# Kernel optimization log

Hardware: AMD Instinct MI355X
Metric: run time of the kernel (lower is better)

The kernel has to match this reference:

```python
import jax, jax.numpy as jnp
import numpy as np

NUM_HEADS = 8
ATTN_DIM = 64

def setup_inputs() -> dict:
    key = jax.random.key(0)
    ks = jax.random.split(key, 16)
    C = ATTN_DIM
    inp = {
        "rgb_fea": jax.random.normal(ks[0], (2, C, 48, 48), jnp.float32),
        "depth_fea": jax.random.normal(ks[1], (2, 1, 24, 24), jnp.float32),
        # expend_conv: Conv2d(1 -> C, k=1), with bias (torch default)
        "w_exp": jax.random.normal(ks[2], (C, 1), jnp.float32) * 0.2,
        "b_exp": jax.random.normal(ks[3], (C,), jnp.float32) * 0.02,
        # q/k/v linears (no bias), weights stored torch-style [out, in]
        "w_rgb_q": jax.random.normal(ks[4], (C, C), jnp.float32) * (C ** -0.5),
        "w_rgb_k": jax.random.normal(ks[5], (C, C), jnp.float32) * (C ** -0.5),
        "w_rgb_v": jax.random.normal(ks[6], (C, C), jnp.float32) * (C ** -0.5),
        "w_dep_q": jax.random.normal(ks[7], (C, C), jnp.float32) * (C ** -0.5),
        "w_dep_k": jax.random.normal(ks[8], (C, C), jnp.float32) * (C ** -0.5),
        "w_dep_v": jax.random.normal(ks[9], (C, C), jnp.float32) * (C ** -0.5),
        # output projections (with bias)
        "w_rgb_proj": jax.random.normal(ks[10], (C, C), jnp.float32) * (C ** -0.5),
        "b_rgb_proj": jax.random.normal(ks[11], (C,), jnp.float32) * 0.02,
        "w_dep_proj": jax.random.normal(ks[12], (C, C), jnp.float32) * (C ** -0.5),
        "b_dep_proj": jax.random.normal(ks[13], (C,), jnp.float32) * 0.02,
        # compress_conv: Conv2d(2C -> C, k=1), with bias
        "w_comp": jax.random.normal(ks[14], (C, 2 * C), jnp.float32) * ((2 * C) ** -0.5),
        "b_comp": jax.random.normal(ks[15], (C,), jnp.float32) * 0.02,
    }
    return inp


def _heads(x, b, n, h):
    # [B, N, C] -> [B, H, N, C/H]
    c = x.shape[-1]
    return x.reshape(b, n, h, c // h).transpose(0, 2, 1, 3)


def reference(rgb_fea, depth_fea, w_exp, b_exp,
              w_rgb_q, w_rgb_k, w_rgb_v, w_dep_q, w_dep_k, w_dep_v,
              w_rgb_proj, b_rgb_proj, w_dep_proj, b_dep_proj,
              w_comp, b_comp):
    b, c, h, w = rgb_fea.shape
    H = NUM_HEADS
    scale = (c // H) ** -0.5

    # expend_conv (1x1) + ReLU + bilinear upsample (align_corners=False)
    d = jnp.einsum('bihw,oi->bohw', depth_fea, w_exp) + b_exp[None, :, None, None]
    d = jax.nn.relu(d)
    d = jax.image.resize(d, (b, c, h, w), method='bilinear')

    # (B,C,H,W) -> transpose(1,3) -> (B,W,H,C) -> (B, N=w*h, C)
    N = w * h
    rgb = rgb_fea.transpose(0, 3, 2, 1).reshape(b, N, c)
    dep = d.transpose(0, 3, 2, 1).reshape(b, N, c)

    rq = _heads(rgb @ w_rgb_q.T, b, N, H)
    rk = _heads(rgb @ w_rgb_k.T, b, N, H)
    rv = _heads(rgb @ w_rgb_v.T, b, N, H)
    dq = _heads(dep @ w_dep_q.T, b, N, H)
    dk = _heads(dep @ w_dep_k.T, b, N, H)
    dv = _heads(dep @ w_dep_v.T, b, N, H)

    # rgb queries attend to depth keys/values
    rgb_attn = jax.nn.softmax(jnp.einsum('bhnd,bhmd->bhnm', rq, dk) * scale, axis=-1)
    rgb_out = jnp.einsum('bhnm,bhmd->bhnd', rgb_attn, dv)
    rgb_out = rgb_out.transpose(0, 2, 1, 3).reshape(b, N, c) @ w_rgb_proj.T + b_rgb_proj

    # depth queries attend to rgb keys/values
    dep_attn = jax.nn.softmax(jnp.einsum('bhnd,bhmd->bhnm', dq, rk) * scale, axis=-1)
    dep_out = jnp.einsum('bhnm,bhmd->bhnd', dep_attn, rv)
    dep_out = dep_out.transpose(0, 2, 1, 3).reshape(b, N, c) @ w_dep_proj.T + b_dep_proj

    # (B,N,C) -> (B,C,N) -> (B,C,w,h)
    rgb_out = rgb_out.transpose(0, 2, 1).reshape(b, c, w, h)
    dep_out = dep_out.transpose(0, 2, 1).reshape(b, c, w, h)

    fuse = jnp.concatenate([rgb_out, dep_out], axis=1)
    fuse = jnp.einsum('bihw,oi->bohw', fuse, w_comp) + b_comp[None, :, None, None]
    return jax.nn.gelu(fuse, approximate=False)
```

## Files before the change

kernel.cpp:

```cpp
#include <hip/hip_runtime.h>
#include <math.h>

#define BATCH 2
#define C 64
#define HH 48
#define WW 48
#define NTOK 2304
#define HEADS 8
#define KVSTRIDE 12

typedef unsigned short bf16_t;
typedef __attribute__((ext_vector_type(8))) short bf16x8;
typedef __attribute__((ext_vector_type(4))) float f32x4;

__device__ __forceinline__ bf16_t f2bf(float f) {
    unsigned int u = __float_as_uint(f);
    u = (u + 0x7fffu + ((u >> 16) & 1u)) >> 16;
    return (bf16_t)u;
}
__device__ __forceinline__ unsigned pack2(float a, float b) {
    return (unsigned)f2bf(a) | ((unsigned)f2bf(b) << 16);
}
__device__ __forceinline__ float4 ld_bf4(const bf16_t* p) {
    uint2 v = *(const uint2*)p;
    float4 r;
    r.x = __uint_as_float(v.x << 16); r.y = __uint_as_float(v.x & 0xffff0000u);
    r.z = __uint_as_float(v.y << 16); r.w = __uint_as_float(v.y & 0xffff0000u);
    return r;
}

__device__ __forceinline__ void stage_x_row(
    float* xrow, const float* rgb, const float* dep,
    const float* w_exp, const float* b_exp,
    int b, int n, int strm, int c0, int cstep)
{
    int wi = n / HH, hi = n % HH;
    if (strm == 0) {
        const float* base = rgb + (size_t)b * C * NTOK + (size_t)hi * WW + wi;
        for (int c = c0; c < 64; c += cstep)
            xrow[c] = base[(size_t)c * NTOK];
    } else {
        float cy = 0.5f * hi - 0.25f, cx = 0.5f * wi - 0.25f;
        float fy0 = floorf(cy), fx0 = floorf(cx);
        float fy = cy - fy0, fx = cx - fx0;
        int y0 = max((int)fy0, 0), x0 = max((int)fx0, 0);
        int y1 = min((int)fy0 + 1, 23), x1 = min((int)fx0 + 1, 23);
        const float* dp = dep + b * 576;
        float d00 = dp[y0*24 + x0], d01 = dp[y0*24 + x1];
        float d10 = dp[y1*24 + x0], d11 = dp[y1*24 + x1];
        for (int c = c0; c < 64; c += cstep) {
            float w = w_exp[c], bb = b_exp[c];
            float r00 = fmaxf(w*d00 + bb, 0.f), r01 = fmaxf(w*d01 + bb, 0.f);
            float r10 = fmaxf(w*d10 + bb, 0.f), r11 = fmaxf(w*d11 + bb, 0.f);
            xrow[c] = (1.f-fy)*((1.f-fx)*r00 + fx*r01) + fy*((1.f-fx)*r10 + fx*r11);
        }
    }
}


__global__ __launch_bounds__(256) void wprep_kernel(
    const float* __restrict__ w_rp, const float* __restrict__ w_dp,
    const float* __restrict__ w_comp,
    const float* __restrict__ b_rp, const float* __restrict__ b_dp,
    const float* __restrict__ b_comp,
    float* __restrict__ W1, float* __restrict__ W2, float* __restrict__ beff)
{
    int bx = blockIdx.x, m = blockIdx.y;
    const float* Wp = m ? w_dp : w_rp;
    float* Wo = m ? W2 : W1;
    __shared__ float Wps[64][68];
    int tid = threadIdx.x;
    int sr = tid >> 4, sc4 = (tid & 15) * 4;
    #pragma unroll
    for (int rr = 0; rr < 4; ++rr) {
        int r = rr*16 + sr;
        *(float4*)&Wps[r][sc4] = *(const float4*)&Wp[r*64 + sc4];
    }
    __syncthreads();
    int r = tid >> 4;
    int o = bx*16 + r;
    int c4 = (tid & 15) * 4;
    float a0 = 0, a1 = 0, a2 = 0, a3 = 0;
    for (int j = 0; j < 64; ++j) {
        float wc = w_comp[o*128 + m*64 + j];
        float4 wp = *(const float4*)&Wps[j][c4];
        a0 += wc*wp.x; a1 += wc*wp.y; a2 += wc*wp.z; a3 += wc*wp.w;
    }
    Wo[o*64 + c4]     = a0;
    Wo[o*64 + c4 + 1] = a1;
    Wo[o*64 + c4 + 2] = a2;
    Wo[o*64 + c4 + 3] = a3;
    if (bx == 0 && m == 0 && tid < 64) {
        float s = b_comp[tid];
        for (int j = 0; j < 64; ++j)
            s += w_comp[tid*128 + j] * b_rp[j] + w_comp[tid*128 + 64 + j] * b_dp[j];
        beff[tid] = s;
    }
}

__global__ __launch_bounds__(256) void qkv_kernel(
    const float* __restrict__ rgb, const float* __restrict__ dep,
    const float* __restrict__ w_exp, const float* __restrict__ b_exp,
    const float* __restrict__ w_rq, const float* __restrict__ w_rk, const float* __restrict__ w_rv,
    const float* __restrict__ w_dq, const float* __restrict__ w_dk, const float* __restrict__ w_dv,
    bf16_t* __restrict__ Qb, bf16_t* __restrict__ Kb, bf16_t* __restrict__ VT)
{
    int tile = blockIdx.x;
    int z    = blockIdx.y;
    int b = z >> 1, strm = z & 1;
    int sb = strm*2 + b;

    __shared__ float Xs[64][68];
    __shared__ float Ws[64][68];
    int tid = threadIdx.x;
    {
        int r = tid & 63, c0 = tid >> 6;
        stage_x_row(&Xs[r][0], rgb, dep, w_exp, b_exp, b, tile*64 + r, strm, c0, 4);
    }
    int sr = tid >> 4, sc = (tid & 15) * 4;
    int ty = tid >> 4, tx = tid & 15;

    #pragma unroll
    for (int m = 0; m < 3; ++m) {
        const float* W = strm ? (m == 0 ? w_dq : m == 1 ? w_dk : w_dv)
                              : (m == 0 ? w_rq : m == 1 ? w_rk : w_rv);
        __syncthreads();
        #pragma unroll
        for (int rr = 0; rr < 4; ++rr) {
            int r = rr*16 + sr;
            *(float4*)&Ws[r][sc] = *(const float4*)&W[r*64 + sc];
        }
        __syncthreads();

        float acc[4][4] = {};
        #pragma unroll
        for (int k = 0; k < 64; k += 4) {
            float4 xv[4], wv4[4];
            #pragma unroll
            for (int i = 0; i < 4; ++i) xv[i] = *(const float4*)&Xs[4*ty + i][k];
            #pragma unroll
            for (int j = 0; j < 4; ++j) wv4[j] = *(const float4*)&Ws[tx + 16*j][k];
            #pragma unroll
            for (int i = 0; i < 4; ++i)
                #pragma unroll
                for (int j = 0; j < 4; ++j)
                    acc[i][j] += xv[i].x*wv4[j].x + xv[i].y*wv4[j].y + xv[i].z*wv4[j].z + xv[i].w*wv4[j].w;
        }
        float scale = (m == 0) ? (0.35355339059327373f * 1.4426950408889634f) : 1.0f;
        #pragma unroll
        for (int j = 0; j < 4; ++j) {
            int o = tx + 16*j;
            int h = o >> 3, d = o & 7;
            #pragma unroll
            for (int i = 0; i < 4; ++i) {
                int n = tile*64 + 4*ty + i;
                bf16_t v = f2bf(acc[i][j] * scale);
                if (m == 0)      Qb[(((size_t)sb*8 + h)*NTOK + n)*8 + d] = v;
                else if (m == 1) Kb[(((size_t)sb*8 + h)*NTOK + n)*8 + d] = v;
                else             VT[(((size_t)sb*8 + h)*8 + d)*NTOK + n] = v;
            }
        }
    }
}

__global__ __launch_bounds__(256) void attn_kernel(
    const bf16_t* __restrict__ Qb, const bf16_t* __restrict__ Kb,
    const bf16_t* __restrict__ VT,
    float* __restrict__ AOr, float* __restrict__ AOd)
{
    int h = blockIdx.y;
    int z = blockIdx.z;
    int b = z >> 1, which = z & 1;
    int qsb = which * 2 + b;
    int ksb = (1 - which) * 2 + b;
    const bf16_t* Q  = Qb + ((size_t)qsb * 8 + h) * NTOK * 8;
    const bf16_t* K  = Kb + ((size_t)ksb * 8 + h) * NTOK * 8;
    const bf16_t* Vt = VT + ((size_t)ksb * 8 + h) * 8 * NTOK;
    float* AO = which ? AOd : AOr;

    __shared__ __align__(16) bf16_t Pls[4][16][40];
    __shared__ __align__(16) float  Ols[4][16][16];

    int tid = threadIdx.x;
    int t = tid & 63, w = tid >> 6;
    int m16 = t & 15, quad = t >> 4;
    int qt = blockIdx.x * 4 + w;
    int n0 = qt * 16;

    const bf16x8 zf = {0,0,0,0,0,0,0,0};
    const bf16x8 onesf = {0x3F80,0x3F80,0x3F80,0x3F80,0x3F80,0x3F80,0x3F80,0x3F80};
    const f32x4 cz = {0.f, 0.f, 0.f, 0.f};

    bf16x8 qf = (quad == 0) ? *(const bf16x8*)&Q[(size_t)(n0 + m16) * 8] : zf;

    f32x4 oacc = cz;

    #pragma unroll 1
    for (int ck = 0; ck < 72; ++ck) {
        int k0 = ck * 32;
        bf16x8 kf0 = (quad == 0) ? *(const bf16x8*)&K[(size_t)(k0 + m16) * 8]      : zf;
        bf16x8 kf1 = (quad == 0) ? *(const bf16x8*)&K[(size_t)(k0 + 16 + m16) * 8] : zf;
        bf16x8 vf = (m16 < 8) ? *(const bf16x8*)&Vt[(size_t)m16 * NTOK + k0 + quad * 8]
                  : (m16 == 8 ? onesf : zf);

        f32x4 s0 = __builtin_amdgcn_mfma_f32_16x16x32_bf16(qf, kf0, cz, 0, 0, 0);
        f32x4 s1 = __builtin_amdgcn_mfma_f32_16x16x32_bf16(qf, kf1, cz, 0, 0, 0);

        #pragma unroll
        for (int r = 0; r < 4; ++r) {
            float p0 = __builtin_amdgcn_exp2f(s0[r]);
            float p1 = __builtin_amdgcn_exp2f(s1[r]);
            Pls[w][quad*4 + r][m16]      = (bf16_t)(__float_as_uint(p0) >> 16);
            Pls[w][quad*4 + r][m16 + 16] = (bf16_t)(__float_as_uint(p1) >> 16);
        }
        bf16x8 pf = *(const bf16x8*)&Pls[w][m16][quad * 8];
        oacc = __builtin_amdgcn_mfma_f32_16x16x32_bf16(pf, vf, oacc, 0, 0, 0);
    }

    #pragma unroll
    for (int r = 0; r < 4; ++r)
        Ols[w][quad*4 + r][m16] = oacc[r];
    #pragma unroll
    for (int e = 0; e < 2; ++e) {
        int idx = t * 2 + e;
        int qq = idx >> 3, d = idx & 7;
        float val = Ols[w][qq][d] / Ols[w][qq][8];
        AO[((size_t)b * NTOK + n0 + qq) * 64 + 8 * h + d] = val;
    }
}

__global__ __launch_bounds__(256) void outcomp_kernel(
    const float* __restrict__ AOr, const float* __restrict__ AOd,
    const float* __restrict__ W1, const float* __restrict__ W2,
    const float* __restrict__ beff, float* __restrict__ out)
{
    int tile = blockIdx.x;
    int b    = blockIdx.y;
    int n0 = tile * 32;
    __shared__ float Ar[32][68];
    __shared__ float Ad[32][68];
    __shared__ float W1s[64][68];
    __shared__ float W2s[64][68];
    int tid = threadIdx.x;
    #pragma unroll
    for (int pass = 0; pass < 2; ++pass) {
        int idx = tid + pass*256;
        int row = idx >> 4, c4 = (idx & 15) * 4;
        *(float4*)&Ar[row][c4] = *(const float4*)&AOr[((size_t)b*NTOK + n0 + row)*64 + c4];
        *(float4*)&Ad[row][c4] = *(const float4*)&AOd[((size_t)b*NTOK + n0 + row)*64 + c4];
    }
    {
        int sr = tid >> 4, sc4 = (tid & 15) * 4;
        #pragma unroll
        for (int rr = 0; rr < 4; ++rr) {
            int r = rr*16 + sr;
            *(float4*)&W1s[r][sc4] = *(const float4*)&W1[r*64 + sc4];
            *(float4*)&W2s[r][sc4] = *(const float4*)&W2[r*64 + sc4];
        }
    }
    __syncthreads();

    int tx = tid & 15, ty = tid >> 4;
    float g[2][4] = {};
    #pragma unroll
    for (int k = 0; k < 64; k += 4) {
        float4 xr0 = *(const float4*)&Ar[2*ty][k];
        float4 xr1 = *(const float4*)&Ar[2*ty + 1][k];
        float4 xd0 = *(const float4*)&Ad[2*ty][k];
        float4 xd1 = *(const float4*)&Ad[2*ty + 1][k];
        #pragma unroll
        for (int jj = 0; jj < 4; ++jj) {
            float4 w1 = *(const float4*)&W1s[tx + 16*jj][k];
            float4 w2 = *(const float4*)&W2s[tx + 16*jj][k];
            g[0][jj] += xr0.x*w1.x + xr0.y*w1.y + xr0.z*w1.z + xr0.w*w1.w
                      + xd0.x*w2.x + xd0.y*w2.y + xd0.z*w2.z + xd0.w*w2.w;
            g[1][jj] += xr1.x*w1.x + xr1.y*w1.y + xr1.z*w1.z + xr1.w*w1.w
                      + xd1.x*w2.x + xd1.y*w2.y + xd1.z*w2.z + xd1.w*w2.w;
        }
    }
    #pragma unroll
    for (int jj = 0; jj < 4; ++jj) {
        int o = tx + 16*jj;
        float be = beff[o];
        #pragma unroll
        for (int i = 0; i < 2; ++i) {
            int n = n0 + 2*ty + i;
            int wi = n / HH, hi = n % HH;
            float x = g[i][jj] + be;
            float gl = 0.5f * x * (1.0f + erff(x * 0.70710678118654752f));
            out[((b*C + o)*WW + wi)*HH + hi] = gl;
        }
    }
}

__global__ __launch_bounds__(256) void kv_all_kernel(
    const float* __restrict__ rgb, const float* __restrict__ dep,
    const float* __restrict__ w_exp, const float* __restrict__ b_exp,
    const float* __restrict__ w_rk, const float* __restrict__ w_rv,
    const float* __restrict__ w_dk, const float* __restrict__ w_dv,
    bf16_t* __restrict__ Kr, bf16_t* __restrict__ Vr,
    bf16_t* __restrict__ Kd, bf16_t* __restrict__ Vd)
{
    int tile = blockIdx.x;
    int m    = blockIdx.y;
    int z    = blockIdx.z;
    int b = z >> 1, strm = z & 1;
    const float* W = strm ? (m ? w_dv : w_dk) : (m ? w_rv : w_rk);
    bf16_t* O = (strm ? (m ? Vd : Kd) : (m ? Vr : Kr))
              + ((size_t)b * NTOK + tile * 64) * 64;

    __shared__ float Xs[64][68];
    __shared__ float Ws[64][68];
    int tid = threadIdx.x;
    {
        int r = tid & 63, c0 = tid >> 6;
        stage_x_row(&Xs[r][0], rgb, dep, w_exp, b_exp, b, tile*64 + r, strm, c0, 4);
    }
    int sr = tid >> 4, sc = (tid & 15) * 4;
    #pragma unroll
    for (int rr = 0; rr < 4; ++rr) {
        int r = rr*16 + sr;
        *(float4*)&Ws[r][sc] = *(const float4*)&W[r*64 + sc];
    }
    __syncthreads();

    int ty = tid >> 4, tx = tid & 15;
    float acc[4][4] = {};
    #pragma unroll
    for (int k = 0; k < 64; k += 4) {
        float4 xv[4], wv4[4];
        #pragma unroll
        for (int i = 0; i < 4; ++i) xv[i] = *(const float4*)&Xs[4*ty + i][k];
        #pragma unroll
        for (int j = 0; j < 4; ++j) wv4[j] = *(const float4*)&Ws[tx + 16*j][k];
        #pragma unroll
        for (int i = 0; i < 4; ++i)
            #pragma unroll
            for (int j = 0; j < 4; ++j)
                acc[i][j] += xv[i].x*wv4[j].x + xv[i].y*wv4[j].y + xv[i].z*wv4[j].z + xv[i].w*wv4[j].w;
    }
    #pragma unroll
    for (int i = 0; i < 4; ++i)
        #pragma unroll
        for (int j = 0; j < 4; ++j)
            O[(4*ty + i)*64 + tx + 16*j] = f2bf(acc[i][j]);
}

__global__ __launch_bounds__(256) void attn_all_kernel(
    const float* __restrict__ rgb, const float* __restrict__ dep,
    const float* __restrict__ w_exp, const float* __restrict__ b_exp,
    const float* __restrict__ w_rq, const float* __restrict__ w_dq,
    const bf16_t* __restrict__ Kr, const bf16_t* __restrict__ Vr,
    const bf16_t* __restrict__ Kd, const bf16_t* __restrict__ Vd,
    bf16_t* __restrict__ AOr, bf16_t* __restrict__ AOd)
{
    int qt = blockIdx.x;
    int h  = blockIdx.y;
    int z  = blockIdx.z;
    int b = z >> 1, which = z & 1;
    const float* wq = which ? w_dq : w_rq;
    const bf16_t* K = which ? Kr : Kd;
    const bf16_t* V = which ? Vr : Vd;
    bf16_t* AO      = which ? AOd : AOr;

    __shared__ float Xs[64][68];
    __shared__ float Wqs[8][64];
    __shared__ __align__(16) float Ks[4][64][KVSTRIDE];
    __shared__ __align__(16) float Vs[4][64][KVSTRIDE];

    int tid = threadIdx.x;
    int t = tid & 63;
    int w = tid >> 6;
    int n = qt * 64 + t;

    stage_x_row(&Xs[t][0], rgb, dep, w_exp, b_exp, b, n, which == 0 ? 0 : 1, w, 4);
    if (w == 0) {
        #pragma unroll
        for (int d = 0; d < 8; ++d) Wqs[d][t] = wq[(8*h + d)*64 + t];
    }
    __syncthreads();

    const float sc = 0.35355339059327373f * 1.4426950408889634f;
    float q[8];
    #pragma unroll
    for (int d = 0; d < 8; ++d) {
        float s = 0.f;
        #pragma unroll 8
        for (int c = 0; c < 64; ++c) s += Xs[t][c] * Wqs[d][c];
        q[d] = s * sc;
    }

    float mrun = -INFINITY, l = 0.f;
    float acc[8] = {};

    #pragma unroll 1
    for (int st = 0; st < 9; ++st) {
        __syncthreads();
        {
            size_t g = ((size_t)b * NTOK + (w*576 + st*64 + t)) * 64 + 8 * h;
            *(float4*)&Ks[w][t][0] = ld_bf4(&K[g]);
            *(float4*)&Ks[w][t][4] = ld_bf4(&K[g + 4]);
            *(float4*)&Vs[w][t][0] = ld_bf4(&V[g]);
            *(float4*)&Vs[w][t][4] = ld_bf4(&V[g + 4]);
        }
        __syncthreads();

        for (int g8 = 0; g8 < 8; ++g8) {
            float s[8];
            #pragma unroll
            for (int u = 0; u < 8; ++u) {
                const float4 ka = *(const float4*)&Ks[w][g8*8 + u][0];
                const float4 kb = *(const float4*)&Ks[w][g8*8 + u][4];
                s[u] = q[0]*ka.x + q[1]*ka.y + q[2]*ka.z + q[3]*ka.w
                     + q[4]*kb.x + q[5]*kb.y + q[6]*kb.z + q[7]*kb.w;
            }
            float tm = fmaxf(fmaxf(fmaxf(s[0],s[1]), fmaxf(s[2],s[3])),
                             fmaxf(fmaxf(s[4],s[5]), fmaxf(s[6],s[7])));
            float mn = fmaxf(mrun, tm);
            float alpha = __builtin_amdgcn_exp2f(mrun - mn);
            float ps = 0.f;
            #pragma unroll
            for (int u = 0; u < 8; ++u) { s[u] = __builtin_amdgcn_exp2f(s[u] - mn); ps += s[u]; }
            l = l * alpha + ps;
            #pragma unroll
            for (int d = 0; d < 8; ++d) acc[d] *= alpha;
            #pragma unroll
            for (int u = 0; u < 8; ++u) {
                const float4 va = *(const float4*)&Vs[w][g8*8 + u][0];
                const float4 vb = *(const float4*)&Vs[w][g8*8 + u][4];
                acc[0] += s[u]*va.x; acc[1] += s[u]*va.y; acc[2] += s[u]*va.z; acc[3] += s[u]*va.w;
                acc[4] += s[u]*vb.x; acc[5] += s[u]*vb.y; acc[6] += s[u]*vb.z; acc[7] += s[u]*vb.w;
            }
            mrun = mn;
        }
    }

    float* part = &Xs[0][0];
    __syncthreads();
    {
        float* p = &part[(w*64 + t) * 10];
        p[0] = mrun; p[1] = l;
        #pragma unroll
        for (int d = 0; d < 8; ++d) p[2 + d] = acc[d];
    }
    __syncthreads();
    if (tid < 64) {
        float M = -INFINITY;
        #pragma unroll
        for (int v = 0; v < 4; ++v) M = fmaxf(M, part[(v*64 + t)*10]);
        float L = 0.f, o[8] = {};
        #pragma unroll
        for (int v = 0; v < 4; ++v) {
            const float* p = &part[(v*64 + t)*10];
            float al = __builtin_amdgcn_exp2f(p[0] - M);
            L += p[1] * al;
            #pragma unroll
            for (int d = 0; d < 8; ++d) o[d] += p[2 + d] * al;
        }
        float inv = 1.0f / L;
        uint4 ov;
        ov.x = pack2(o[0]*inv, o[1]*inv);
        ov.y = pack2(o[2]*inv, o[3]*inv);
        ov.z = pack2(o[4]*inv, o[5]*inv);
        ov.w = pack2(o[6]*inv, o[7]*inv);
        *(uint4*)&AO[((size_t)b * NTOK + n) * 64 + 8 * h] = ov;
    }
}

__global__ __launch_bounds__(256) void projcomp_all_kernel(
    const bf16_t* __restrict__ AOr, const bf16_t* __restrict__ AOd,
    const float* __restrict__ w_rp, const float* __restrict__ b_rp,
    const float* __restrict__ w_dp, const float* __restrict__ b_dp,
    const float* __restrict__ w_comp, const float* __restrict__ b_comp,
    float* __restrict__ out)
{
    int tile = blockIdx.x;
    int b    = blockIdx.y;
    __shared__ float A[64][68];
    __shared__ float Bf[64][68];
    __shared__ float Pf[64][68];
    int tid = threadIdx.x;
    int sr = tid >> 4, sc = (tid & 15) * 4;
    int ty = tid >> 4, tx = tid & 15;
    float G[4][4] = {};

    #pragma unroll
    for (int half = 0; half < 2; ++half) {
        const bf16_t* AOx = half ? AOd : AOr;
        const float* Wp   = half ? w_dp : w_rp;
        const float* bp   = half ? b_dp : b_rp;
        #pragma unroll
        for (int rr = 0; rr < 4; ++rr) {
            int r = rr*16 + sr;
            *(float4*)&A[r][sc]  = ld_bf4(&AOx[((size_t)b*NTOK + tile*64 + r)*64 + sc]);
            *(float4*)&Bf[r][sc] = *(const float4*)&Wp[r*64 + sc];
        }
        __syncthreads();
        float acc[4][4] = {};
        #pragma unroll
        for (int k = 0; k < 64; k += 4) {
            float4 xv[4], wv[4];
            #pragma unroll
            for (int i = 0; i < 4; ++i) xv[i] = *(const float4*)&A[4*ty + i][k];
            #pragma unroll
            for (int j = 0; j < 4; ++j) wv[j] = *(const float4*)&Bf[tx + 16*j][k];
            #pragma unroll
            for (int i = 0; i < 4; ++i)
                #pragma unroll
                for (int j = 0; j < 4; ++j)
                    acc[i][j] += xv[i].x*wv[j].x + xv[i].y*wv[j].y + xv[i].z*wv[j].z + xv[i].w*wv[j].w;
        }
        __syncthreads();
        #pragma unroll
        for (int j = 0; j < 4; ++j) {
            float bj = bp[tx + 16*j];
            #pragma unroll
            for (int i = 0; i < 4; ++i)
                Pf[4*ty + i][tx + 16*j] = acc[i][j] + bj;
        }
        #pragma unroll
        for (int rr = 0; rr < 4; ++rr) {
            int r = rr*16 + sr;
            *(float4*)&Bf[r][sc] = *(const float4*)&w_comp[r*128 + half*64 + sc];
        }
        __syncthreads();
        #pragma unroll
        for (int k = 0; k < 64; k += 4) {
            float4 xv[4], wv[4];
            #pragma unroll
            for (int i = 0; i < 4; ++i) xv[i] = *(const float4*)&Pf[4*ty + i][k];
            #pragma unroll
            for (int j = 0; j < 4; ++j) wv[j] = *(const float4*)&Bf[tx + 16*j][k];
            #pragma unroll
            for (int i = 0; i < 4; ++i)
                #pragma unroll
                for (int j = 0; j < 4; ++j)
                    G[i][j] += xv[i].x*wv[j].x + xv[i].y*wv[j].y + xv[i].z*wv[j].z + xv[i].w*wv[j].w;
        }
        __syncthreads();
    }

    #pragma unroll
    for (int j = 0; j < 4; ++j) {
        int o = tx + 16*j;
        float bj = b_comp[o];
        #pragma unroll
        for (int i = 0; i < 4; ++i) {
            int n = tile*64 + 4*ty + i;
            int wi = n / HH, hi = n % HH;
            float x = G[i][j] + bj;
            float g = 0.5f * x * (1.0f + erff(x * 0.70710678118654752f));
            out[((b*C + o)*WW + wi)*HH + hi] = g;
        }
    }
}

extern "C" void kernel_launch(void* const* d_in, const int* in_sizes, int n_in,
                              void* d_out, int out_size, void* d_ws, size_t ws_size,
                              hipStream_t stream) {
    const float* rgb_fea = (const float*)d_in[0];
    const float* depth   = (const float*)d_in[1];
    const float* w_exp   = (const float*)d_in[2];
    const float* b_exp   = (const float*)d_in[3];
    const float* w_rq    = (const float*)d_in[4];
    const float* w_rk    = (const float*)d_in[5];
    const float* w_rv    = (const float*)d_in[6];
    const float* w_dq    = (const float*)d_in[7];
    const float* w_dk    = (const float*)d_in[8];
    const float* w_dv    = (const float*)d_in[9];
    const float* w_rp    = (const float*)d_in[10];
    const float* b_rp    = (const float*)d_in[11];
    const float* w_dp    = (const float*)d_in[12];
    const float* b_dp    = (const float*)d_in[13];
    const float* w_comp  = (const float*)d_in[14];
    const float* b_comp  = (const float*)d_in[15];
    float* out = (float*)d_out;

    if (ws_size >= 5931264) {
        char* Wb = (char*)d_ws;
        bf16_t* Qb  = (bf16_t*)Wb;
        bf16_t* Kb  = (bf16_t*)(Wb + 1179648);
        bf16_t* VT  = (bf16_t*)(Wb + 2359296);
        float* AOr  = (float*)(Wb + 3538944);
        float* AOd  = (float*)(Wb + 4718592);
        float* W1   = (float*)(Wb + 5898240);
        float* W2   = (float*)(Wb + 5914624);
        float* beff = (float*)(Wb + 5931008);

        wprep_kernel<<<dim3(4, 2), dim3(256), 0, stream>>>(
            w_rp, w_dp, w_comp, b_rp, b_dp, b_comp, W1, W2, beff);
        qkv_kernel<<<dim3(36, 4), dim3(256), 0, stream>>>(
            rgb_fea, depth, w_exp, b_exp,
            w_rq, w_rk, w_rv, w_dq, w_dk, w_dv, Qb, Kb, VT);
        attn_kernel<<<dim3(36, 8, 4), dim3(256), 0, stream>>>(
            Qb, Kb, VT, AOr, AOd);
        outcomp_kernel<<<dim3(72, 2), dim3(256), 0, stream>>>(
            AOr, AOd, W1, W2, beff, out);
    } else {
        const size_t BUF = (size_t)BATCH * NTOK * 64;
        bf16_t* Kr  = (bf16_t*)d_ws;
        bf16_t* Vr  = Kr + BUF;
        bf16_t* Kd  = Vr + BUF;
        bf16_t* Vd  = Kd + BUF;
        bf16_t* AOr = Vd + BUF;
        bf16_t* AOd = AOr + BUF;
        kv_all_kernel<<<dim3(36, 2, 4), dim3(256), 0, stream>>>(
            rgb_fea, depth, w_exp, b_exp, w_rk, w_rv, w_dk, w_dv, Kr, Vr, Kd, Vd);
        attn_all_kernel<<<dim3(36, 8, 4), dim3(256), 0, stream>>>(
            rgb_fea, depth, w_exp, b_exp, w_rq, w_dq, Kr, Vr, Kd, Vd, AOr, AOd);
        projcomp_all_kernel<<<dim3(36, 2), dim3(256), 0, stream>>>(
            AOr, AOd, w_rp, b_rp, w_dp, b_dp, w_comp, b_comp, out);
    }
}
```

Before: 191.2 us.

## Split input staging into transpose prep kernel, halve QKV tile, coalesce output stores

Adds an xprep kernel that transposes the rgb features through shared memory and computes the depth expand, ReLU and bilinear upsample once into a token-major buffer. The QKV kernel then loads rows with float4 reads and uses 32-token tiles, doubling the grid to 288 blocks. The output kernel stages its GELU results in shared memory so the final stores to the output are coalesced float4 writes. In exchange this adds a kernel launch and an extra round trip of the staged features through global memory, reusing the AOr region as scratch.

```diff
diff --git a/kernel.cpp b/kernel.cpp
--- a/kernel.cpp
+++ b/kernel.cpp
@@ -98,9 +98,72 @@
     }
 }
 
-__global__ __launch_bounds__(256) void qkv_kernel(
+__global__ __launch_bounds__(256) void xprep_kernel(
     const float* __restrict__ rgb, const float* __restrict__ dep,
     const float* __restrict__ w_exp, const float* __restrict__ b_exp,
+    float* __restrict__ Xt)
+{
+    int t = blockIdx.x;
+    int z = blockIdx.y;
+    int b = z >> 1, strm = z & 1;
+    __shared__ float Ls[64][65];
+    int tid = threadIdx.x;
+
+    if (strm == 0) {
+        const float* src = rgb + (size_t)b * C * NTOK + t * 64;
+        #pragma unroll
+        for (int p = 0; p < 4; ++p) {
+            int idx = tid + p * 256;
+            int c = idx >> 4, m4 = (idx & 15) * 4;
+            *(float4*)&Ls[c][m4] = *(const float4*)&src[(size_t)c * NTOK + m4];
+        }
+        __syncthreads();
+        #pragma unroll
+        for (int p = 0; p < 4; ++p) {
+            int idx = tid + p * 256;
+            int row = idx >> 4, l = idx & 15;
+            int mi = t * 64 + row;
+            int hi = mi / 48, wi = mi % 48;
+            int n  = wi * 48 + hi;
+            float4 v;
+            v.x = Ls[4*l + 0][row];
+            v.y = Ls[4*l + 1][row];
+            v.z = Ls[4*l + 2][row];
+            v.w = Ls[4*l + 3][row];
+            *(float4*)&Xt[((size_t)z * NTOK + n) * 64 + 4*l] = v;
+        }
+    } else {
+        int tok_l = tid >> 2, cq = (tid & 3) * 16;
+        int n = t * 64 + tok_l;
+        int wi = n / HH, hi = n % HH;
+        float cy = 0.5f * hi - 0.25f, cx = 0.5f * wi - 0.25f;
+        float fy0 = floorf(cy), fx0 = floorf(cx);
+        float fy = cy - fy0, fx = cx - fx0;
+        int y0 = max((int)fy0, 0), x0 = max((int)fx0, 0);
+        int y1 = min((int)fy0 + 1, 23), x1 = min((int)fx0 + 1, 23);
+        const float* dp = dep + b * 576;
+        float d00 = dp[y0*24 + x0], d01 = dp[y0*24 + x1];
+        float d10 = dp[y1*24 + x0], d11 = dp[y1*24 + x1];
+        float* orow = &Xt[((size_t)z * NTOK + n) * 64];
+        #pragma unroll
+        for (int cc = 0; cc < 16; cc += 4) {
+            float4 v;
+            #pragma unroll
+            for (int j = 0; j < 4; ++j) {
+                int c = cq + cc + j;
+                float w = w_exp[c], bb = b_exp[c];
+                float r00 = fmaxf(w*d00 + bb, 0.f), r01 = fmaxf(w*d01 + bb, 0.f);
+                float r10 = fmaxf(w*d10 + bb, 0.f), r11 = fmaxf(w*d11 + bb, 0.f);
+                float val = (1.f-fy)*((1.f-fx)*r00 + fx*r01) + fy*((1.f-fx)*r10 + fx*r11);
+                ((float*)&v)[j] = val;
+            }
+            *(float4*)&orow[cq + cc] = v;
+        }
+    }
+}
+
+__global__ __launch_bounds__(256) void qkv_kernel(
+    const float* __restrict__ Xt,
     const float* __restrict__ w_rq, const float* __restrict__ w_rk, const float* __restrict__ w_rv,
     const float* __restrict__ w_dq, const float* __restrict__ w_dk, const float* __restrict__ w_dv,
     bf16_t* __restrict__ Qb, bf16_t* __restrict__ Kb, bf16_t* __restrict__ VT)
@@ -110,12 +173,14 @@
     int b = z >> 1, strm = z & 1;
     int sb = strm*2 + b;
 
-    __shared__ float Xs[64][68];
+    __shared__ float Xs[32][68];
     __shared__ float Ws[64][68];
     int tid = threadIdx.x;
-    {
-        int r = tid & 63, c0 = tid >> 6;
-        stage_x_row(&Xs[r][0], rgb, dep, w_exp, b_exp, b, tile*64 + r, strm, c0, 4);
+    #pragma unroll
+    for (int p = 0; p < 2; ++p) {
+        int idx = tid + p*256;
+        int r = idx >> 4, c4 = (idx & 15) * 4;
+        *(float4*)&Xs[r][c4] = *(const float4*)&Xt[((size_t)z*NTOK + tile*32 + r)*64 + c4];
     }
     int sr = tid >> 4, sc = (tid & 15) * 4;
     int ty = tid >> 4, tx = tid & 15;
@@ -132,16 +197,16 @@
         }
         __syncthreads();
 
-        float acc[4][4] = {};
+        float acc[2][4] = {};
         #pragma unroll
         for (int k = 0; k < 64; k += 4) {
-            float4 xv[4], wv4[4];
-            #pragma unroll
-            for (int i = 0; i < 4; ++i) xv[i] = *(const float4*)&Xs[4*ty + i][k];
+            float4 xv[2], wv4[4];
+            #pragma unroll
+            for (int i = 0; i < 2; ++i) xv[i] = *(const float4*)&Xs[2*ty + i][k];
             #pragma unroll
             for (int j = 0; j < 4; ++j) wv4[j] = *(const float4*)&Ws[tx + 16*j][k];
             #pragma unroll
-            for (int i = 0; i < 4; ++i)
+            for (int i = 0; i < 2; ++i)
                 #pragma unroll
                 for (int j = 0; j < 4; ++j)
                     acc[i][j] += xv[i].x*wv4[j].x + xv[i].y*wv4[j].y + xv[i].z*wv4[j].z + xv[i].w*wv4[j].w;
@@ -152,8 +217,8 @@
             int o = tx + 16*j;
             int h = o >> 3, d = o & 7;
             #pragma unroll
-            for (int i = 0; i < 4; ++i) {
-                int n = tile*64 + 4*ty + i;
+            for (int i = 0; i < 2; ++i) {
+                int n = tile*32 + 2*ty + i;
                 bf16_t v = f2bf(acc[i][j] * scale);
                 if (m == 0)      Qb[(((size_t)sb*8 + h)*NTOK + n)*8 + d] = v;
                 else if (m == 1) Kb[(((size_t)sb*8 + h)*NTOK + n)*8 + d] = v;
@@ -278,18 +343,27 @@
                       + xd1.x*w2.x + xd1.y*w2.y + xd1.z*w2.z + xd1.w*w2.w;
         }
     }
+
+    __syncthreads();
+    float* Gs = &W1s[0][0];
     #pragma unroll
     for (int jj = 0; jj < 4; ++jj) {
         int o = tx + 16*jj;
         float be = beff[o];
         #pragma unroll
         for (int i = 0; i < 2; ++i) {
-            int n = n0 + 2*ty + i;
-            int wi = n / HH, hi = n % HH;
             float x = g[i][jj] + be;
             float gl = 0.5f * x * (1.0f + erff(x * 0.70710678118654752f));
-            out[((b*C + o)*WW + wi)*HH + hi] = gl;
-        }
+            Gs[o*40 + 2*ty + i] = gl;
+        }
+    }
+    __syncthreads();
+    #pragma unroll
+    for (int p = 0; p < 2; ++p) {
+        int idx = tid + p*256;
+        int o = idx >> 3, s = idx & 7;
+        float4 v = *(const float4*)&Gs[o*40 + 4*s];
+        *(float4*)&out[((size_t)(b*C + o))*NTOK + n0 + 4*s] = v;
     }
 }
 
@@ -586,12 +660,14 @@
         float* W1   = (float*)(Wb + 5898240);
         float* W2   = (float*)(Wb + 5914624);
         float* beff = (float*)(Wb + 5931008);
+        float* Xt   = (float*)(Wb + 3538944);
 
         wprep_kernel<<<dim3(4, 2), dim3(256), 0, stream>>>(
             w_rp, w_dp, w_comp, b_rp, b_dp, b_comp, W1, W2, beff);
-        qkv_kernel<<<dim3(36, 4), dim3(256), 0, stream>>>(
-            rgb_fea, depth, w_exp, b_exp,
-            w_rq, w_rk, w_rv, w_dq, w_dk, w_dv, Qb, Kb, VT);
+        xprep_kernel<<<dim3(36, 4), dim3(256), 0, stream>>>(
+            rgb_fea, depth, w_exp, b_exp, Xt);
+        qkv_kernel<<<dim3(72, 4), dim3(256), 0, stream>>>(
+            Xt, w_rq, w_rk, w_rv, w_dq, w_dk, w_dv, Qb, Kb, VT);
         attn_kernel<<<dim3(36, 8, 4), dim3(256), 0, stream>>>(
             Qb, Kb, VT, AOr, AOd);
         outcomp_kernel<<<dim3(72, 2), dim3(256), 0, stream>>>(
```

After: 190.7 us. No clear change (-0.3%).

## Fuse attention with output projection and merge weight prep into QKV kernel

Applied to the files above, without the earlier changes.

Merges the weight-folding work into the QKV projection kernel as extra blocks, and fuses attention with the combined projection, compress conv and GELU in one kernel. Each block now handles 16 queries for all heads and both directions, so the per-head attention outputs stay in shared memory instead of going to global memory. The key loop also processes 64 keys per iteration for more instruction-level parallelism, and the output store is staged through shared memory so it writes coalesced. This removes two launches and the intermediate global buffers, but cuts the grid to 288 blocks where each wave runs four heads in sequence, which lowers occupancy and parallelism on the attention part.

```diff
diff --git a/kernel.cpp b/kernel.cpp
--- a/kernel.cpp
+++ b/kernel.cpp
@@ -58,238 +58,235 @@
 }
 
 
-__global__ __launch_bounds__(256) void wprep_kernel(
+__global__ __launch_bounds__(256) void qkvprep_kernel(
+    const float* __restrict__ rgb, const float* __restrict__ dep,
+    const float* __restrict__ w_exp, const float* __restrict__ b_exp,
+    const float* __restrict__ w_rq, const float* __restrict__ w_rk,
+    const float* __restrict__ w_rv,
+    const float* __restrict__ w_dq, const float* __restrict__ w_dk,
+    const float* __restrict__ w_dv,
     const float* __restrict__ w_rp, const float* __restrict__ w_dp,
     const float* __restrict__ w_comp,
     const float* __restrict__ b_rp, const float* __restrict__ b_dp,
     const float* __restrict__ b_comp,
+    bf16_t* __restrict__ Qb, bf16_t* __restrict__ Kb, bf16_t* __restrict__ VT,
     float* __restrict__ W1, float* __restrict__ W2, float* __restrict__ beff)
 {
-    int bx = blockIdx.x, m = blockIdx.y;
-    const float* Wp = m ? w_dp : w_rp;
-    float* Wo = m ? W2 : W1;
-    __shared__ float Wps[64][68];
-    int tid = threadIdx.x;
-    int sr = tid >> 4, sc4 = (tid & 15) * 4;
-    #pragma unroll
-    for (int rr = 0; rr < 4; ++rr) {
-        int r = rr*16 + sr;
-        *(float4*)&Wps[r][sc4] = *(const float4*)&Wp[r*64 + sc4];
-    }
-    __syncthreads();
-    int r = tid >> 4;
-    int o = bx*16 + r;
-    int c4 = (tid & 15) * 4;
-    float a0 = 0, a1 = 0, a2 = 0, a3 = 0;
-    for (int j = 0; j < 64; ++j) {
-        float wc = w_comp[o*128 + m*64 + j];
-        float4 wp = *(const float4*)&Wps[j][c4];
-        a0 += wc*wp.x; a1 += wc*wp.y; a2 += wc*wp.z; a3 += wc*wp.w;
-    }
-    Wo[o*64 + c4]     = a0;
-    Wo[o*64 + c4 + 1] = a1;
-    Wo[o*64 + c4 + 2] = a2;
-    Wo[o*64 + c4 + 3] = a3;
-    if (bx == 0 && m == 0 && tid < 64) {
-        float s = b_comp[tid];
-        for (int j = 0; j < 64; ++j)
-            s += w_comp[tid*128 + j] * b_rp[j] + w_comp[tid*128 + 64 + j] * b_dp[j];
-        beff[tid] = s;
-    }
-}
-
-__global__ __launch_bounds__(256) void qkv_kernel(
-    const float* __restrict__ rgb, const float* __restrict__ dep,
-    const float* __restrict__ w_exp, const float* __restrict__ b_exp,
-    const float* __restrict__ w_rq, const float* __restrict__ w_rk, const float* __restrict__ w_rv,
-    const float* __restrict__ w_dq, const float* __restrict__ w_dk, const float* __restrict__ w_dv,
-    bf16_t* __restrict__ Qb, bf16_t* __restrict__ Kb, bf16_t* __restrict__ VT)
-{
-    int tile = blockIdx.x;
-    int z    = blockIdx.y;
-    int b = z >> 1, strm = z & 1;
-    int sb = strm*2 + b;
-
     __shared__ float Xs[64][68];
     __shared__ float Ws[64][68];
+    int bid = blockIdx.x;
     int tid = threadIdx.x;
-    {
-        int r = tid & 63, c0 = tid >> 6;
-        stage_x_row(&Xs[r][0], rgb, dep, w_exp, b_exp, b, tile*64 + r, strm, c0, 4);
-    }
-    int sr = tid >> 4, sc = (tid & 15) * 4;
-    int ty = tid >> 4, tx = tid & 15;
-
-    #pragma unroll
-    for (int m = 0; m < 3; ++m) {
-        const float* W = strm ? (m == 0 ? w_dq : m == 1 ? w_dk : w_dv)
-                              : (m == 0 ? w_rq : m == 1 ? w_rk : w_rv);
-        __syncthreads();
+
+    if (bid < 144) {
+        int tile = bid % 36, z = bid / 36;
+        int b = z >> 1, strm = z & 1;
+        int sb = strm*2 + b;
+        {
+            int r = tid & 63, c0 = tid >> 6;
+            stage_x_row(&Xs[r][0], rgb, dep, w_exp, b_exp, b, tile*64 + r, strm, c0, 4);
+        }
+        int sr = tid >> 4, sc = (tid & 15) * 4;
+        int ty = tid >> 4, tx = tid & 15;
+
+        #pragma unroll
+        for (int m = 0; m < 3; ++m) {
+            const float* W = strm ? (m == 0 ? w_dq : m == 1 ? w_dk : w_dv)
+                                  : (m == 0 ? w_rq : m == 1 ? w_rk : w_rv);
+            __syncthreads();
+            #pragma unroll
+            for (int rr = 0; rr < 4; ++rr) {
+                int r = rr*16 + sr;
+                *(float4*)&Ws[r][sc] = *(const float4*)&W[r*64 + sc];
+            }
+            __syncthreads();
+
+            float acc[4][4] = {};
+            #pragma unroll
+            for (int k = 0; k < 64; k += 4) {
+                float4 xv[4], wv4[4];
+                #pragma unroll
+                for (int i = 0; i < 4; ++i) xv[i] = *(const float4*)&Xs[4*ty + i][k];
+                #pragma unroll
+                for (int j = 0; j < 4; ++j) wv4[j] = *(const float4*)&Ws[tx + 16*j][k];
+                #pragma unroll
+                for (int i = 0; i < 4; ++i)
+                    #pragma unroll
+                    for (int j = 0; j < 4; ++j)
+                        acc[i][j] += xv[i].x*wv4[j].x + xv[i].y*wv4[j].y
+                                   + xv[i].z*wv4[j].z + xv[i].w*wv4[j].w;
+            }
+            float scale = (m == 0) ? (0.35355339059327373f * 1.4426950408889634f) : 1.0f;
+            #pragma unroll
+            for (int j = 0; j < 4; ++j) {
+                int o = tx + 16*j;
+                int h = o >> 3, d = o & 7;
+                #pragma unroll
+                for (int i = 0; i < 4; ++i) {
+                    int n = tile*64 + 4*ty + i;
+                    bf16_t v = f2bf(acc[i][j] * scale);
+                    if (m == 0)      Qb[(((size_t)sb*8 + h)*NTOK + n)*8 + d] = v;
+                    else if (m == 1) Kb[(((size_t)sb*8 + h)*NTOK + n)*8 + d] = v;
+                    else             VT[(((size_t)sb*8 + h)*8 + d)*NTOK + n] = v;
+                }
+            }
+        }
+    } else {
+        int idx0 = bid - 144;
+        int bx = idx0 & 3, m = idx0 >> 2;
+        const float* Wp = m ? w_dp : w_rp;
+        float* Wo = m ? W2 : W1;
+        int sr = tid >> 4, sc4 = (tid & 15) * 4;
         #pragma unroll
         for (int rr = 0; rr < 4; ++rr) {
             int r = rr*16 + sr;
-            *(float4*)&Ws[r][sc] = *(const float4*)&W[r*64 + sc];
+            *(float4*)&Xs[r][sc4] = *(const float4*)&Wp[r*64 + sc4];
         }
         __syncthreads();
-
-        float acc[4][4] = {};
-        #pragma unroll
-        for (int k = 0; k < 64; k += 4) {
-            float4 xv[4], wv4[4];
-            #pragma unroll
-            for (int i = 0; i < 4; ++i) xv[i] = *(const float4*)&Xs[4*ty + i][k];
-            #pragma unroll
-            for (int j = 0; j < 4; ++j) wv4[j] = *(const float4*)&Ws[tx + 16*j][k];
-            #pragma unroll
-            for (int i = 0; i < 4; ++i)
-                #pragma unroll
-                for (int j = 0; j < 4; ++j)
-                    acc[i][j] += xv[i].x*wv4[j].x + xv[i].y*wv4[j].y + xv[i].z*wv4[j].z + xv[i].w*wv4[j].w;
-        }
-        float scale = (m == 0) ? (0.35355339059327373f * 1.4426950408889634f) : 1.0f;
-        #pragma unroll
-        for (int j = 0; j < 4; ++j) {
-            int o = tx + 16*j;
-            int h = o >> 3, d = o & 7;
-            #pragma unroll
-            for (int i = 0; i < 4; ++i) {
-                int n = tile*64 + 4*ty + i;
-                bf16_t v = f2bf(acc[i][j] * scale);
-                if (m == 0)      Qb[(((size_t)sb*8 + h)*NTOK + n)*8 + d] = v;
-                else if (m == 1) Kb[(((size_t)sb*8 + h)*NTOK + n)*8 + d] = v;
-                else             VT[(((size_t)sb*8 + h)*8 + d)*NTOK + n] = v;
-            }
-        }
-    }
-}
-
-__global__ __launch_bounds__(256) void attn_kernel(
+        int r = tid >> 4;
+        int o = bx*16 + r;
+        int c4 = (tid & 15) * 4;
+        float a0 = 0, a1 = 0, a2 = 0, a3 = 0;
+        for (int j = 0; j < 64; ++j) {
+            float wc = w_comp[o*128 + m*64 + j];
+            float4 wp = *(const float4*)&Xs[j][c4];
+            a0 += wc*wp.x; a1 += wc*wp.y; a2 += wc*wp.z; a3 += wc*wp.w;
+        }
+        Wo[o*64 + c4]     = a0;
+        Wo[o*64 + c4 + 1] = a1;
+        Wo[o*64 + c4 + 2] = a2;
+        Wo[o*64 + c4 + 3] = a3;
+        if (bx == 0 && m == 0 && tid < 64) {
+            float s = b_comp[tid];
+            for (int j = 0; j < 64; ++j)
+                s += w_comp[tid*128 + j] * b_rp[j] + w_comp[tid*128 + 64 + j] * b_dp[j];
+            beff[tid] = s;
+        }
+    }
+}
+
+__global__ __launch_bounds__(256) void attnout_kernel(
     const bf16_t* __restrict__ Qb, const bf16_t* __restrict__ Kb,
     const bf16_t* __restrict__ VT,
-    float* __restrict__ AOr, float* __restrict__ AOd)
-{
-    int h = blockIdx.y;
-    int z = blockIdx.z;
-    int b = z >> 1, which = z & 1;
-    int qsb = which * 2 + b;
-    int ksb = (1 - which) * 2 + b;
-    const bf16_t* Q  = Qb + ((size_t)qsb * 8 + h) * NTOK * 8;
-    const bf16_t* K  = Kb + ((size_t)ksb * 8 + h) * NTOK * 8;
-    const bf16_t* Vt = VT + ((size_t)ksb * 8 + h) * 8 * NTOK;
-    float* AO = which ? AOd : AOr;
-
-    __shared__ __align__(16) bf16_t Pls[4][16][40];
-    __shared__ __align__(16) float  Ols[4][16][16];
-
-    int tid = threadIdx.x;
-    int t = tid & 63, w = tid >> 6;
-    int m16 = t & 15, quad = t >> 4;
-    int qt = blockIdx.x * 4 + w;
-    int n0 = qt * 16;
-
-    const bf16x8 zf = {0,0,0,0,0,0,0,0};
-    const bf16x8 onesf = {0x3F80,0x3F80,0x3F80,0x3F80,0x3F80,0x3F80,0x3F80,0x3F80};
-    const f32x4 cz = {0.f, 0.f, 0.f, 0.f};
-
-    bf16x8 qf = (quad == 0) ? *(const bf16x8*)&Q[(size_t)(n0 + m16) * 8] : zf;
-
-    f32x4 oacc = cz;
-
-    #pragma unroll 1
-    for (int ck = 0; ck < 72; ++ck) {
-        int k0 = ck * 32;
-        bf16x8 kf0 = (quad == 0) ? *(const bf16x8*)&K[(size_t)(k0 + m16) * 8]      : zf;
-        bf16x8 kf1 = (quad == 0) ? *(const bf16x8*)&K[(size_t)(k0 + 16 + m16) * 8] : zf;
-        bf16x8 vf = (m16 < 8) ? *(const bf16x8*)&Vt[(size_t)m16 * NTOK + k0 + quad * 8]
-                  : (m16 == 8 ? onesf : zf);
-
-        f32x4 s0 = __builtin_amdgcn_mfma_f32_16x16x32_bf16(qf, kf0, cz, 0, 0, 0);
-        f32x4 s1 = __builtin_amdgcn_mfma_f32_16x16x32_bf16(qf, kf1, cz, 0, 0, 0);
-
-        #pragma unroll
-        for (int r = 0; r < 4; ++r) {
-            float p0 = __builtin_amdgcn_exp2f(s0[r]);
-            float p1 = __builtin_amdgcn_exp2f(s1[r]);
-            Pls[w][quad*4 + r][m16]      = (bf16_t)(__float_as_uint(p0) >> 16);
-            Pls[w][quad*4 + r][m16 + 16] = (bf16_t)(__float_as_uint(p1) >> 16);
-        }
-        bf16x8 pf = *(const bf16x8*)&Pls[w][m16][quad * 8];
-        oacc = __builtin_amdgcn_mfma_f32_16x16x32_bf16(pf, vf, oacc, 0, 0, 0);
-    }
-
-    #pragma unroll
-    for (int r = 0; r < 4; ++r)
-        Ols[w][quad*4 + r][m16] = oacc[r];
-    #pragma unroll
-    for (int e = 0; e < 2; ++e) {
-        int idx = t * 2 + e;
-        int qq = idx >> 3, d = idx & 7;
-        float val = Ols[w][qq][d] / Ols[w][qq][8];
-        AO[((size_t)b * NTOK + n0 + qq) * 64 + 8 * h + d] = val;
-    }
-}
-
-__global__ __launch_bounds__(256) void outcomp_kernel(
-    const float* __restrict__ AOr, const float* __restrict__ AOd,
     const float* __restrict__ W1, const float* __restrict__ W2,
     const float* __restrict__ beff, float* __restrict__ out)
 {
-    int tile = blockIdx.x;
-    int b    = blockIdx.y;
-    int n0 = tile * 32;
-    __shared__ float Ar[32][68];
-    __shared__ float Ad[32][68];
-    __shared__ float W1s[64][68];
-    __shared__ float W2s[64][68];
+    __shared__ __align__(16) bf16_t Pls[4][2][16][40];
+    __shared__ __align__(16) float  Ols[4][16][16];
+    __shared__ __align__(16) float  AOls[2][16][68];
+    __shared__ __align__(16) float  Wsh[2][64][68];
+
+    int bid = blockIdx.x;
     int tid = threadIdx.x;
-    #pragma unroll
-    for (int pass = 0; pass < 2; ++pass) {
-        int idx = tid + pass*256;
-        int row = idx >> 4, c4 = (idx & 15) * 4;
-        *(float4*)&Ar[row][c4] = *(const float4*)&AOr[((size_t)b*NTOK + n0 + row)*64 + c4];
-        *(float4*)&Ad[row][c4] = *(const float4*)&AOd[((size_t)b*NTOK + n0 + row)*64 + c4];
-    }
+    int tile = bid % 144, b = bid / 144;
+    int n0 = tile * 16;
+
     {
         int sr = tid >> 4, sc4 = (tid & 15) * 4;
         #pragma unroll
         for (int rr = 0; rr < 4; ++rr) {
             int r = rr*16 + sr;
-            *(float4*)&W1s[r][sc4] = *(const float4*)&W1[r*64 + sc4];
-            *(float4*)&W2s[r][sc4] = *(const float4*)&W2[r*64 + sc4];
+            *(float4*)&Wsh[0][r][sc4] = *(const float4*)&W1[r*64 + sc4];
+            *(float4*)&Wsh[1][r][sc4] = *(const float4*)&W2[r*64 + sc4];
+        }
+    }
+
+    int t = tid & 63, w = tid >> 6;
+    int m16 = t & 15, quad = t >> 4;
+    const bf16x8 zf = {0,0,0,0,0,0,0,0};
+    const bf16x8 onesf = {0x3F80,0x3F80,0x3F80,0x3F80,
+                          0x3F80,0x3F80,0x3F80,0x3F80};
+    const f32x4 cz = {0.f, 0.f, 0.f, 0.f};
+    bf16_t* PA = &Pls[w][0][0][0];
+    bf16_t* PB = &Pls[w][1][0][0];
+
+    #pragma unroll 1
+    for (int i = 0; i < 4; ++i) {
+        int unit = w * 4 + i;
+        int which = unit >> 3, h = unit & 7;
+        int qsb = which * 2 + b;
+        int ksb = (1 - which) * 2 + b;
+        const bf16_t* Q  = Qb + ((size_t)qsb * 8 + h) * NTOK * 8;
+        const bf16_t* K  = Kb + ((size_t)ksb * 8 + h) * NTOK * 8;
+        const bf16_t* Vt = VT + ((size_t)ksb * 8 + h) * 8 * NTOK;
+
+        bf16x8 qf = (quad == 0) ? *(const bf16x8*)&Q[(size_t)(n0 + m16) * 8] : zf;
+        f32x4 oacc = cz;
+
+        #pragma unroll 1
+        for (int cc = 0; cc < 36; ++cc) {
+            int k0 = cc * 64;
+            bf16x8 kA0 = (quad == 0) ? *(const bf16x8*)&K[(size_t)(k0 + m16) * 8]      : zf;
+            bf16x8 kA1 = (quad == 0) ? *(const bf16x8*)&K[(size_t)(k0 + 16 + m16) * 8] : zf;
+            bf16x8 kB0 = (quad == 0) ? *(const bf16x8*)&K[(size_t)(k0 + 32 + m16) * 8] : zf;
+            bf16x8 kB1 = (quad == 0) ? *(const bf16x8*)&K[(size_t)(k0 + 48 + m16) * 8] : zf;
+            bf16x8 vA = (m16 < 8) ? *(const bf16x8*)&Vt[(size_t)m16 * NTOK + k0 + quad * 8]
+                      : (m16 == 8 ? onesf : zf);
+            bf16x8 vB = (m16 < 8) ? *(const bf16x8*)&Vt[(size_t)m16 * NTOK + k0 + 32 + quad * 8]
+                      : (m16 == 8 ? onesf : zf);
+
+            f32x4 sA0 = __builtin_amdgcn_mfma_f32_16x16x32_bf16(qf, kA0, cz, 0, 0, 0);
+            f32x4 sA1 = __builtin_amdgcn_mfma_f32_16x16x32_bf16(qf, kA1, cz, 0, 0, 0);
+            f32x4 sB0 = __builtin_amdgcn_mfma_f32_16x16x32_bf16(qf, kB0, cz, 0, 0, 0);
+            f32x4 sB1 = __builtin_amdgcn_mfma_f32_16x16x32_bf16(qf, kB1, cz, 0, 0, 0);
+
+            #pragma unroll
+            for (int q4 = 0; q4 < 4; ++q4) {
+                float a0 = __builtin_amdgcn_exp2f(sA0[q4]);
+                float a1 = __builtin_amdgcn_exp2f(sA1[q4]);
+                float b0 = __builtin_amdgcn_exp2f(sB0[q4]);
+                float b1 = __builtin_amdgcn_exp2f(sB1[q4]);
+                PA[(quad*4 + q4)*40 + m16]      = (bf16_t)(__float_as_uint(a0) >> 16);
+                PA[(quad*4 + q4)*40 + m16 + 16] = (bf16_t)(__float_as_uint(a1) >> 16);
+                PB[(quad*4 + q4)*40 + m16]      = (bf16_t)(__float_as_uint(b0) >> 16);
+                PB[(quad*4 + q4)*40 + m16 + 16] = (bf16_t)(__float_as_uint(b1) >> 16);
+            }
+            bf16x8 pfA = *(const bf16x8*)&PA[m16*40 + quad * 8];
+            oacc = __builtin_amdgcn_mfma_f32_16x16x32_bf16(pfA, vA, oacc, 0, 0, 0);
+            bf16x8 pfB = *(const bf16x8*)&PB[m16*40 + quad * 8];
+            oacc = __builtin_amdgcn_mfma_f32_16x16x32_bf16(pfB, vB, oacc, 0, 0, 0);
+        }
+
+        #pragma unroll
+        for (int q4 = 0; q4 < 4; ++q4)
+            Ols[w][quad*4 + q4][m16] = oacc[q4];
+        #pragma unroll
+        for (int e = 0; e < 2; ++e) {
+            int idx = t * 2 + e;
+            int qq = idx >> 3, d = idx & 7;
+            AOls[which][qq][8*h + d] = Ols[w][qq][d] / Ols[w][qq][8];
         }
     }
     __syncthreads();
 
     int tx = tid & 15, ty = tid >> 4;
-    float g[2][4] = {};
+    float g[4] = {};
     #pragma unroll
     for (int k = 0; k < 64; k += 4) {
-        float4 xr0 = *(const float4*)&Ar[2*ty][k];
-        float4 xr1 = *(const float4*)&Ar[2*ty + 1][k];
-        float4 xd0 = *(const float4*)&Ad[2*ty][k];
-        float4 xd1 = *(const float4*)&Ad[2*ty + 1][k];
+        float4 xr = *(const float4*)&AOls[0][ty][k];
+        float4 xd = *(const float4*)&AOls[1][ty][k];
         #pragma unroll
         for (int jj = 0; jj < 4; ++jj) {
-            float4 w1 = *(const float4*)&W1s[tx + 16*jj][k];
-            float4 w2 = *(const float4*)&W2s[tx + 16*jj][k];
-            g[0][jj] += xr0.x*w1.x + xr0.y*w1.y + xr0.z*w1.z + xr0.w*w1.w
-                      + xd0.x*w2.x + xd0.y*w2.y + xd0.z*w2.z + xd0.w*w2.w;
-            g[1][jj] += xr1.x*w1.x + xr1.y*w1.y + xr1.z*w1.z + xr1.w*w1.w
-                      + xd1.x*w2.x + xd1.y*w2.y + xd1.z*w2.z + xd1.w*w2.w;
-        }
-    }
+            float4 w1 = *(const float4*)&Wsh[0][tx + 16*jj][k];
+            float4 w2 = *(const float4*)&Wsh[1][tx + 16*jj][k];
+            g[jj] += xr.x*w1.x + xr.y*w1.y + xr.z*w1.z + xr.w*w1.w
+                   + xd.x*w2.x + xd.y*w2.y + xd.z*w2.z + xd.w*w2.w;
+        }
+    }
+
+    __syncthreads();
+    float* Gs = (float*)&Pls[0][0][0][0];
     #pragma unroll
     for (int jj = 0; jj < 4; ++jj) {
         int o = tx + 16*jj;
-        float be = beff[o];
-        #pragma unroll
-        for (int i = 0; i < 2; ++i) {
-            int n = n0 + 2*ty + i;
-            int wi = n / HH, hi = n % HH;
-            float x = g[i][jj] + be;
-            float gl = 0.5f * x * (1.0f + erff(x * 0.70710678118654752f));
-            out[((b*C + o)*WW + wi)*HH + hi] = gl;
-        }
+        float x = g[jj] + beff[o];
+        float gl = 0.5f * x * (1.0f + erff(x * 0.70710678118654752f));
+        Gs[o*20 + ty] = gl;
+    }
+    __syncthreads();
+    {
+        int o = tid >> 2, s = tid & 3;
+        float4 v = *(const float4*)&Gs[o*20 + 4*s];
+        *(float4*)&out[((size_t)(b*C + o))*NTOK + n0 + 4*s] = v;
     }
 }
 
@@ -576,26 +573,22 @@
     const float* b_comp  = (const float*)d_in[15];
     float* out = (float*)d_out;
 
-    if (ws_size >= 5931264) {
+    if (ws_size >= 3571968) {
         char* Wb = (char*)d_ws;
-        bf16_t* Qb  = (bf16_t*)Wb;
-        bf16_t* Kb  = (bf16_t*)(Wb + 1179648);
-        bf16_t* VT  = (bf16_t*)(Wb + 2359296);
-        float* AOr  = (float*)(Wb + 3538944);
-        float* AOd  = (float*)(Wb + 4718592);
-        float* W1   = (float*)(Wb + 5898240);
-        float* W2   = (float*)(Wb + 5914624);
-        float* beff = (float*)(Wb + 5931008);
-
-        wprep_kernel<<<dim3(4, 2), dim3(256), 0, stream>>>(
-            w_rp, w_dp, w_comp, b_rp, b_dp, b_comp, W1, W2, beff);
-        qkv_kernel<<<dim3(36, 4), dim3(256), 0, stream>>>(
+        bf16_t* Qb   = (bf16_t*)Wb;
+        bf16_t* Kb   = (bf16_t*)(Wb + 1179648);
+        bf16_t* VT   = (bf16_t*)(Wb + 2359296);
+        float*  W1   = (float*)(Wb + 3538944);
+        float*  W2   = (float*)(Wb + 3555328);
+        float*  beff = (float*)(Wb + 3571712);
+
+        qkvprep_kernel<<<dim3(152), dim3(256), 0, stream>>>(
             rgb_fea, depth, w_exp, b_exp,
-            w_rq, w_rk, w_rv, w_dq, w_dk, w_dv, Qb, Kb, VT);
-        attn_kernel<<<dim3(36, 8, 4), dim3(256), 0, stream>>>(
-            Qb, Kb, VT, AOr, AOd);
-        outcomp_kernel<<<dim3(72, 2), dim3(256), 0, stream>>>(
-            AOr, AOd, W1, W2, beff, out);
+            w_rq, w_rk, w_rv, w_dq, w_dk, w_dv,
+            w_rp, w_dp, w_comp, b_rp, b_dp, b_comp,
+            Qb, Kb, VT, W1, W2, beff);
+        attnout_kernel<<<dim3(288), dim3(256), 0, stream>>>(
+            Qb, Kb, VT, W1, W2, beff, out);
     } else {
         const size_t BUF = (size_t)BATCH * NTOK * 64;
         bf16_t* Kr  = (bf16_t*)d_ws;
```

Result: slower. 269.3 us (+40.8%).
